# Kernel optimization log

Hardware: AMD Instinct MI355X
Metric: run time of the kernel (lower is better)

The kernel has to match this reference:

```python
import jax, jax.numpy as jnp
import numpy as np

NUM_NODES = 100000
D_IN = 64
D_OUT = 64
NUM_EDGES = 1200000


def setup_inputs() -> dict:
    key = jax.random.key(0)
    k1, k2, k3, k4 = jax.random.split(key, 4)
    features = jax.random.normal(k1, (NUM_NODES, D_IN), dtype=jnp.float32)
    edge_index = jax.random.randint(k2, (2, NUM_EDGES), 0, NUM_NODES, dtype=jnp.int64)
    # Linear(input_dim*2 -> output_dim) parameters
    W = jax.random.normal(k3, (2 * D_IN, D_OUT), dtype=jnp.float32) / np.sqrt(2 * D_IN)
    b = jax.random.normal(k4, (D_OUT,), dtype=jnp.float32) * 0.01
    return {"features": features, "edge_index": edge_index, "W": W, "b": b}


def reference(features, edge_index, W, b):
    num_nodes = features.shape[0]
    src, dst = edge_index[0], edge_index[1]
    # gather source-node features for every edge: [E, D]
    src_feats = features[src]
    # segment-sum into destination nodes (mean aggregation)
    neigh_sum = jax.ops.segment_sum(src_feats, dst, num_segments=num_nodes)
    degree = jax.ops.segment_sum(jnp.ones_like(dst, dtype=features.dtype), dst,
                                 num_segments=num_nodes)
    degree = jnp.clip(degree, 1.0)
    neigh_mean = neigh_sum / degree[:, None]
    # concat self + neighbor features, then linear (dropout = identity in eval)
    combined = jnp.concatenate([features, neigh_mean], axis=-1)
    return combined @ W + b
```

## Files before the change

### kernel.cpp

```cpp
#include <hip/hip_runtime.h>
#include <hip/hip_fp8.h>

#define N_NODES 100000
#define D 64
#define N_EDGES 1200000
#define NCB 391
#define NBLK 256
#define PAD 16
#define CHUNK ((N_EDGES + NBLK - 1) / NBLK)
#define CSR2 768

typedef __attribute__((ext_vector_type(8))) short short8v;
typedef __attribute__((ext_vector_type(4))) float f32x4;

__device__ __forceinline__ unsigned short f2bf(float x) {
    unsigned int b = __float_as_uint(x);
    b += 0x7FFFu + ((b >> 16) & 1u);
    return (unsigned short)(b >> 16);
}
__device__ __forceinline__ unsigned char ftofp8(float x) {
    __hip_fp8_e4m3 q(x);
    return (unsigned char)q.__x;
}
#if __has_builtin(__builtin_amdgcn_cvt_f32_fp8)
#define F8D(w, s) __builtin_amdgcn_cvt_f32_fp8((w), (s))
#else
__device__ __forceinline__ float f8dec(unsigned int w, unsigned int s) {
    __hip_fp8_e4m3 q; q.__x = (unsigned char)(w >> (8 * s));
    return (float)q;
}
#define F8D(w, s) f8dec((w), (s))
#endif

__global__ __launch_bounds__(256) void bin_hist(
    const int* __restrict__ eidx, int* __restrict__ hist, int* __restrict__ totP,
    const float* __restrict__ feat, unsigned char* __restrict__ f8b,
    const float* __restrict__ W, ushort* __restrict__ wb)
{
    __shared__ int h[NCB];
    for (int i = threadIdx.x; i < NCB; i += 256) h[i] = 0;
    __syncthreads();
    const int blk = blockIdx.x;

    if (blk < 32) {
        int g  = blk * 256 + threadIdx.x;
        int j  = g & 7;
        int l  = (g >> 3) & 63;
        int c4 = (g >> 9) & 3;
        int tt = g >> 11;
        int k   = 32 * tt + ((l >> 4) << 3) + j;
        int col = 16 * c4 + (l & 15);
        wb[g] = f2bf(W[k * 64 + col]);
    }

    const int beg = blk * CHUNK;
    const int end = min(beg + CHUNK, N_EDGES);
    for (int e = beg + threadIdx.x; e < end; e += 256)
        atomicAdd(&h[eidx[N_EDGES + e] >> 8], 1);

    const int total4 = N_NODES * D / 4;
    for (int i = blk * 256 + threadIdx.x; i < total4; i += NBLK * 256) {
        float4 v = ((const float4*)feat)[i];
        uchar4 o;
        o.x = ftofp8(v.x); o.y = ftofp8(v.y); o.z = ftofp8(v.z); o.w = ftofp8(v.w);
        ((uchar4*)f8b)[i] = o;
    }

    __syncthreads();
    for (int i = threadIdx.x; i < NCB; i += 256) {
        int v = h[i];
        hist[blk * NCB + i] = v;
        if (v) atomicAdd(&totP[i * PAD], v);
    }
}

__global__ __launch_bounds__(256) void rstart(
    const int* __restrict__ totP, const int* __restrict__ hist,
    int* __restrict__ boff, int* __restrict__ runstart)
{
    __shared__ int red[256];
    __shared__ int pfx[256];
    __shared__ int bo_s;

    const int tid = threadIdx.x;
    const int i   = blockIdx.x;

    int p = 0;
    for (int j = tid; j < i; j += 256) p += totP[j * PAD];
    red[tid] = p;
    __syncthreads();
    for (int off = 128; off > 0; off >>= 1) {
        if (tid < off) red[tid] += red[tid + off];
        __syncthreads();
    }
    if (tid == 0) {
        bo_s = red[0];
        boff[i] = red[0];
        if (i == 0) boff[NCB] = N_EDGES;
    }
    __syncthreads();

    int v = hist[tid * NCB + i];
    pfx[tid] = v;
    __syncthreads();
    for (int off = 1; off < 256; off <<= 1) {
        int x = (tid >= off) ? pfx[tid - off] : 0;
        __syncthreads();
        pfx[tid] += x;
        __syncthreads();
    }
    runstart[tid * NCB + i] = bo_s + pfx[tid] - v;
}

__global__ __launch_bounds__(256) void bin_fill(
    const int* __restrict__ eidx, const int* __restrict__ runstart,
    unsigned int* __restrict__ pairs)
{
    __shared__ int lcur[NCB];
    const int blk = blockIdx.x;
    for (int i = threadIdx.x; i < NCB; i += 256) lcur[i] = runstart[blk * NCB + i];
    __syncthreads();
    const int beg = blk * CHUNK;
    const int end = min(beg + CHUNK, N_EDGES);
    for (int e = beg + threadIdx.x; e < end; e += 256) {
        int src = eidx[e];
        int dst = eidx[N_EDGES + e];
        int pos = atomicAdd(&lcur[dst >> 8], 1);
        pairs[pos] = ((unsigned int)src << 8) | (unsigned int)(dst & 255);
    }
}

#define MROW 72
#define D8X(sel) (((F8D(w0.x,sel)+F8D(w1.x,sel))+(F8D(w2.x,sel)+F8D(w3.x,sel))) \
               + ((F8D(w4.x,sel)+F8D(w5.x,sel))+(F8D(w6.x,sel)+F8D(w7.x,sel))))
#define D8Y(sel) (((F8D(w0.y,sel)+F8D(w1.y,sel))+(F8D(w2.y,sel)+F8D(w3.y,sel))) \
               + ((F8D(w4.y,sel)+F8D(w5.y,sel))+(F8D(w6.y,sel)+F8D(w7.y,sel))))
#define D4X(sel) ((F8D(w0.x,sel)+F8D(w1.x,sel))+(F8D(w2.x,sel)+F8D(w3.x,sel)))
#define D4Y(sel) ((F8D(w0.y,sel)+F8D(w1.y,sel))+(F8D(w2.y,sel)+F8D(w3.y,sel)))
__global__ __launch_bounds__(256) void sage_fused(
    const unsigned char* __restrict__ f8b,
    const float* __restrict__ feat,
    const int* __restrict__ boff,
    const unsigned int* __restrict__ pairs,
    const ushort* __restrict__ wb,
    const float* __restrict__ bias,
    float* __restrict__ out)
{
    __shared__ int cnt[32];
    __shared__ int lofs[33];
    __shared__ int lcur2[32];
    __shared__ int csrL[CSR2];
    __shared__ __attribute__((aligned(16))) ushort means[32 * MROW];

    const int tid = threadIdx.x;
    const int b   = blockIdx.x >> 3;
    const int c   = blockIdx.x & 7;
    const int n0  = b * 256 + c * 32;
    if (n0 >= N_NODES) return;

    const int beg = boff[b];
    const int end = boff[b + 1];

    if (tid < 32) cnt[tid] = 0;
    __syncthreads();
    for (int j = beg + tid; j < end; j += 256) {
        unsigned int p = pairs[j];
        int ld = (int)(p & 255u);
        if ((ld >> 5) == c) atomicAdd(&cnt[ld & 31], 1);
    }
    __syncthreads();
    if (tid == 0) {
        int run = 0;
        #pragma unroll
        for (int k = 0; k < 32; ++k) { lofs[k] = run; run += cnt[k]; }
        lofs[32] = run;
    }
    __syncthreads();
    if (tid < 32) lcur2[tid] = lofs[tid];
    __syncthreads();
    for (int j = beg + tid; j < end; j += 256) {
        unsigned int p = pairs[j];
        int ld = (int)(p & 255u);
        if ((ld >> 5) == c) {
            int pos = atomicAdd(&lcur2[ld & 31], 1);
            if (pos < CSR2) csrL[pos] = (int)(p >> 8);
        }
    }
    __syncthreads();

    const int l    = tid & 7;
    const int node = tid >> 3;

    int ebeg = lofs[node];
    int eend = lofs[node + 1];
    const int deg = eend - ebeg;
    if (ebeg > CSR2) ebeg = CSR2;
    if (eend > CSR2) eend = CSR2;
    const uint2* g8 = (const uint2*)f8b;

    float s0=0.f,s1=0.f,s2=0.f,s3=0.f,s4=0.f,s5=0.f,s6=0.f,s7=0.f;
    int e = ebeg;
    for (; e + 8 <= eend; e += 8) {
        int i0=csrL[e+0], i1=csrL[e+1], i2=csrL[e+2], i3=csrL[e+3];
        int i4=csrL[e+4], i5=csrL[e+5], i6=csrL[e+6], i7=csrL[e+7];
        uint2 w0 = g8[(size_t)i0 * 8 + l];
        uint2 w1 = g8[(size_t)i1 * 8 + l];
        uint2 w2 = g8[(size_t)i2 * 8 + l];
        uint2 w3 = g8[(size_t)i3 * 8 + l];
        uint2 w4 = g8[(size_t)i4 * 8 + l];
        uint2 w5 = g8[(size_t)i5 * 8 + l];
        uint2 w6 = g8[(size_t)i6 * 8 + l];
        uint2 w7 = g8[(size_t)i7 * 8 + l];
        s0 += D8X(0); s1 += D8X(1); s2 += D8X(2); s3 += D8X(3);
        s4 += D8Y(0); s5 += D8Y(1); s6 += D8Y(2); s7 += D8Y(3);
    }
    for (; e + 4 <= eend; e += 4) {
        int i0=csrL[e+0], i1=csrL[e+1], i2=csrL[e+2], i3=csrL[e+3];
        uint2 w0 = g8[(size_t)i0 * 8 + l];
        uint2 w1 = g8[(size_t)i1 * 8 + l];
        uint2 w2 = g8[(size_t)i2 * 8 + l];
        uint2 w3 = g8[(size_t)i3 * 8 + l];
        s0 += D4X(0); s1 += D4X(1); s2 += D4X(2); s3 += D4X(3);
        s4 += D4Y(0); s5 += D4Y(1); s6 += D4Y(2); s7 += D4Y(3);
    }
    for (; e < eend; ++e) {
        uint2 w0 = g8[(size_t)csrL[e] * 8 + l];
        s0 += F8D(w0.x,0); s1 += F8D(w0.x,1); s2 += F8D(w0.x,2); s3 += F8D(w0.x,3);
        s4 += F8D(w0.y,0); s5 += F8D(w0.y,1); s6 += F8D(w0.y,2); s7 += F8D(w0.y,3);
    }

    float dg = (float)deg;
    dg = dg > 1.0f ? dg : 1.0f;
    float inv = 1.0f / dg;
    {
        ushort s[8] = { f2bf(s0*inv), f2bf(s1*inv), f2bf(s2*inv), f2bf(s3*inv),
                        f2bf(s4*inv), f2bf(s5*inv), f2bf(s6*inv), f2bf(s7*inv) };
        *(ushort4*)(means + node * MROW + l * 8)     = *(ushort4*)&s[0];
        *(ushort4*)(means + node * MROW + l * 8 + 4) = *(ushort4*)&s[4];
    }
    __syncthreads();

    const int lane = tid & 63;
    const int wv   = tid >> 6;
    const int rt   = wv >> 1;
    const int cp   = wv & 1;
    const int kg   = lane >> 4;
    const int cl   = lane & 15;

    const float* frow = feat + (size_t)(n0 + rt * 16 + cl) * 64;
    f32x4 p0 = *(const f32x4*)(frow + kg * 8);
    f32x4 p1 = *(const f32x4*)(frow + kg * 8 + 4);
    f32x4 p2 = *(const f32x4*)(frow + 32 + kg * 8);
    f32x4 p3 = *(const f32x4*)(frow + 32 + kg * 8 + 4);
    short8v a0, a1;
    #pragma unroll
    for (int k = 0; k < 4; ++k) {
        a0[k]     = (short)f2bf(p0[k]);
        a0[k + 4] = (short)f2bf(p1[k]);
        a1[k]     = (short)f2bf(p2[k]);
        a1[k + 4] = (short)f2bf(p3[k]);
    }
    const ushort* mrow = means + (rt * 16 + cl) * MROW;
    short8v a2 = *(const short8v*)(mrow + kg * 8);
    short8v a3 = *(const short8v*)(mrow + 32 + kg * 8);

    const short8v* wv8 = (const short8v*)wb;

    #pragma unroll
    for (int qq = 0; qq < 2; ++qq) {
        const int c4 = cp * 2 + qq;
        float bv = bias[c4 * 16 + cl];
        f32x4 acc = (f32x4){bv, bv, bv, bv};
        acc = __builtin_amdgcn_mfma_f32_16x16x32_bf16(
            a0, wv8[(0 * 4 + c4) * 64 + lane], acc, 0, 0, 0);
        acc = __builtin_amdgcn_mfma_f32_16x16x32_bf16(
            a1, wv8[(1 * 4 + c4) * 64 + lane], acc, 0, 0, 0);
        acc = __builtin_amdgcn_mfma_f32_16x16x32_bf16(
            a2, wv8[(2 * 4 + c4) * 64 + lane], acc, 0, 0, 0);
        acc = __builtin_amdgcn_mfma_f32_16x16x32_bf16(
            a3, wv8[(3 * 4 + c4) * 64 + lane], acc, 0, 0, 0);
        #pragma unroll
        for (int r = 0; r < 4; ++r)
            out[(size_t)(n0 + rt * 16 + kg * 4 + r) * 64 + c4 * 16 + cl] = acc[r];
    }
}

extern "C" void kernel_launch(void* const* d_in, const int* in_sizes, int n_in,
                              void* d_out, int out_size, void* d_ws, size_t ws_size,
                              hipStream_t stream) {
    const float* feat = (const float*)d_in[0];
    const int*   eidx = (const int*)d_in[1];
    const float* W    = (const float*)d_in[2];
    const float* bias = (const float*)d_in[3];
    float* out = (float*)d_out;

    int* hist     = (int*)d_ws;
    int* totP     = hist + NBLK * NCB;
    int* runstart = totP + NCB * PAD;
    int* boff     = runstart + NBLK * NCB;
    ushort* wb    = (ushort*)(boff + 396);
    unsigned int* pairs = (unsigned int*)(wb + 8192);
    unsigned char* f8b  = (unsigned char*)(pairs + N_EDGES);

    hipMemsetAsync(totP, 0, (size_t)NCB * PAD * sizeof(int), stream);

    bin_hist<<<NBLK, 256, 0, stream>>>(eidx, hist, totP, feat, f8b, W, wb);
    rstart<<<NCB, 256, 0, stream>>>(totP, hist, boff, runstart);
    bin_fill<<<NBLK, 256, 0, stream>>>(eidx, runstart, pairs);
    sage_fused<<<NCB * 8, 256, 0, stream>>>(f8b, feat, boff, pairs, wb, bias, out);
}
```

Measured before the change: 97.74 us.

## Process each 256-node bin in one 512-thread block instead of eight blocks

The fused aggregation kernel now launches one 512-thread block per 256-node bin, down from eight 256-thread blocks that each rescanned the whole bin's edge pairs and kept only their 32-node slice. The block builds a full 256-entry local CSR once, using a parallel prefix scan, then loops over four 64-node groups doing the gather-mean and the MFMA linear step. This removes the eightfold redundant reading of pairs and the atomics. The cost is a much smaller grid (391 blocks), serialized groups with extra barriers, and more shared memory, which may reduce occupancy and latency hiding.

```diff
diff --git a/kernel.cpp b/kernel.cpp
--- a/kernel.cpp
+++ b/kernel.cpp
@@ -8,7 +8,7 @@
 #define NBLK 256
 #define PAD 16
 #define CHUNK ((N_EDGES + NBLK - 1) / NBLK)
-#define CSR2 768
+#define CSRMAX 3584
 
 typedef __attribute__((ext_vector_type(8))) short short8v;
 typedef __attribute__((ext_vector_type(4))) float f32x4;
@@ -137,7 +137,7 @@
                + ((F8D(w4.y,sel)+F8D(w5.y,sel))+(F8D(w6.y,sel)+F8D(w7.y,sel))))
 #define D4X(sel) ((F8D(w0.x,sel)+F8D(w1.x,sel))+(F8D(w2.x,sel)+F8D(w3.x,sel)))
 #define D4Y(sel) ((F8D(w0.y,sel)+F8D(w1.y,sel))+(F8D(w2.y,sel)+F8D(w3.y,sel)))
-__global__ __launch_bounds__(256) void sage_fused(
+__global__ __launch_bounds__(512) void sage_fused(
     const unsigned char* __restrict__ f8b,
     const float* __restrict__ feat,
     const int* __restrict__ boff,
@@ -146,99 +146,51 @@
     const float* __restrict__ bias,
     float* __restrict__ out)
 {
-    __shared__ int cnt[32];
-    __shared__ int lofs[33];
-    __shared__ int lcur2[32];
-    __shared__ int csrL[CSR2];
-    __shared__ __attribute__((aligned(16))) ushort means[32 * MROW];
-
-    const int tid = threadIdx.x;
-    const int b   = blockIdx.x >> 3;
-    const int c   = blockIdx.x & 7;
-    const int n0  = b * 256 + c * 32;
-    if (n0 >= N_NODES) return;
-
-    const int beg = boff[b];
-    const int end = boff[b + 1];
-
-    if (tid < 32) cnt[tid] = 0;
-    __syncthreads();
-    for (int j = beg + tid; j < end; j += 256) {
+    __shared__ int cnt[256];
+    __shared__ int pfx[256];
+    __shared__ int lofs[257];
+    __shared__ int lcur[256];
+    __shared__ int csrL[CSRMAX];
+    __shared__ __attribute__((aligned(16))) ushort means[64 * MROW];
+
+    const int tid  = threadIdx.x;
+    const int b    = blockIdx.x;
+    const int base = b * 256;
+    const int beg  = boff[b];
+    const int end  = boff[b + 1];
+
+    if (tid < 256) cnt[tid] = 0;
+    __syncthreads();
+    for (int j = beg + tid; j < end; j += 512)
+        atomicAdd(&cnt[pairs[j] & 255], 1);
+    __syncthreads();
+    if (tid < 256) pfx[tid] = cnt[tid];
+    __syncthreads();
+    for (int off = 1; off < 256; off <<= 1) {
+        int x = 0;
+        if (tid < 256 && tid >= off) x = pfx[tid - off];
+        __syncthreads();
+        if (tid < 256) pfx[tid] += x;
+        __syncthreads();
+    }
+    if (tid < 256) {
+        int ex = pfx[tid] - cnt[tid];
+        lofs[tid] = ex;
+        lcur[tid] = ex;
+    }
+    if (tid == 0) lofs[256] = end - beg;
+    __syncthreads();
+    for (int j = beg + tid; j < end; j += 512) {
         unsigned int p = pairs[j];
-        int ld = (int)(p & 255u);
-        if ((ld >> 5) == c) atomicAdd(&cnt[ld & 31], 1);
-    }
-    __syncthreads();
-    if (tid == 0) {
-        int run = 0;
-        #pragma unroll
-        for (int k = 0; k < 32; ++k) { lofs[k] = run; run += cnt[k]; }
-        lofs[32] = run;
-    }
-    __syncthreads();
-    if (tid < 32) lcur2[tid] = lofs[tid];
-    __syncthreads();
-    for (int j = beg + tid; j < end; j += 256) {
-        unsigned int p = pairs[j];
-        int ld = (int)(p & 255u);
-        if ((ld >> 5) == c) {
-            int pos = atomicAdd(&lcur2[ld & 31], 1);
-            if (pos < CSR2) csrL[pos] = (int)(p >> 8);
-        }
+        int pos = atomicAdd(&lcur[p & 255], 1);
+        if (pos < CSRMAX) csrL[pos] = (int)(p >> 8);
     }
     __syncthreads();
 
     const int l    = tid & 7;
-    const int node = tid >> 3;
-
-    int ebeg = lofs[node];
-    int eend = lofs[node + 1];
-    const int deg = eend - ebeg;
-    if (ebeg > CSR2) ebeg = CSR2;
-    if (eend > CSR2) eend = CSR2;
+    const int gn8  = tid >> 3;
     const uint2* g8 = (const uint2*)f8b;
-
-    float s0=0.f,s1=0.f,s2=0.f,s3=0.f,s4=0.f,s5=0.f,s6=0.f,s7=0.f;
-    int e = ebeg;
-    for (; e + 8 <= eend; e += 8) {
-        int i0=csrL[e+0], i1=csrL[e+1], i2=csrL[e+2], i3=csrL[e+3];
-        int i4=csrL[e+4], i5=csrL[e+5], i6=csrL[e+6], i7=csrL[e+7];
-        uint2 w0 = g8[(size_t)i0 * 8 + l];
-        uint2 w1 = g8[(size_t)i1 * 8 + l];
-        uint2 w2 = g8[(size_t)i2 * 8 + l];
-        uint2 w3 = g8[(size_t)i3 * 8 + l];
-        uint2 w4 = g8[(size_t)i4 * 8 + l];
-        uint2 w5 = g8[(size_t)i5 * 8 + l];
-        uint2 w6 = g8[(size_t)i6 * 8 + l];
-        uint2 w7 = g8[(size_t)i7 * 8 + l];
-        s0 += D8X(0); s1 += D8X(1); s2 += D8X(2); s3 += D8X(3);
-        s4 += D8Y(0); s5 += D8Y(1); s6 += D8Y(2); s7 += D8Y(3);
-    }
-    for (; e + 4 <= eend; e += 4) {
-        int i0=csrL[e+0], i1=csrL[e+1], i2=csrL[e+2], i3=csrL[e+3];
-        uint2 w0 = g8[(size_t)i0 * 8 + l];
-        uint2 w1 = g8[(size_t)i1 * 8 + l];
-        uint2 w2 = g8[(size_t)i2 * 8 + l];
-        uint2 w3 = g8[(size_t)i3 * 8 + l];
-        s0 += D4X(0); s1 += D4X(1); s2 += D4X(2); s3 += D4X(3);
-        s4 += D4Y(0); s5 += D4Y(1); s6 += D4Y(2); s7 += D4Y(3);
-    }
-    for (; e < eend; ++e) {
-        uint2 w0 = g8[(size_t)csrL[e] * 8 + l];
-        s0 += F8D(w0.x,0); s1 += F8D(w0.x,1); s2 += F8D(w0.x,2); s3 += F8D(w0.x,3);
-        s4 += F8D(w0.y,0); s5 += F8D(w0.y,1); s6 += F8D(w0.y,2); s7 += F8D(w0.y,3);
-    }
-
-    float dg = (float)deg;
-    dg = dg > 1.0f ? dg : 1.0f;
-    float inv = 1.0f / dg;
-    {
-        ushort s[8] = { f2bf(s0*inv), f2bf(s1*inv), f2bf(s2*inv), f2bf(s3*inv),
-                        f2bf(s4*inv), f2bf(s5*inv), f2bf(s6*inv), f2bf(s7*inv) };
-        *(ushort4*)(means + node * MROW + l * 8)     = *(ushort4*)&s[0];
-        *(ushort4*)(means + node * MROW + l * 8 + 4) = *(ushort4*)&s[4];
-    }
-    __syncthreads();
+    const short8v* wv8 = (const short8v*)wb;
 
     const int lane = tid & 63;
     const int wv   = tid >> 6;
@@ -247,41 +199,98 @@
     const int kg   = lane >> 4;
     const int cl   = lane & 15;
 
-    const float* frow = feat + (size_t)(n0 + rt * 16 + cl) * 64;
-    f32x4 p0 = *(const f32x4*)(frow + kg * 8);
-    f32x4 p1 = *(const f32x4*)(frow + kg * 8 + 4);
-    f32x4 p2 = *(const f32x4*)(frow + 32 + kg * 8);
-    f32x4 p3 = *(const f32x4*)(frow + 32 + kg * 8 + 4);
-    short8v a0, a1;
-    #pragma unroll
-    for (int k = 0; k < 4; ++k) {
-        a0[k]     = (short)f2bf(p0[k]);
-        a0[k + 4] = (short)f2bf(p1[k]);
-        a1[k]     = (short)f2bf(p2[k]);
-        a1[k + 4] = (short)f2bf(p3[k]);
-    }
-    const ushort* mrow = means + (rt * 16 + cl) * MROW;
-    short8v a2 = *(const short8v*)(mrow + kg * 8);
-    short8v a3 = *(const short8v*)(mrow + 32 + kg * 8);
-
-    const short8v* wv8 = (const short8v*)wb;
-
-    #pragma unroll
-    for (int qq = 0; qq < 2; ++qq) {
-        const int c4 = cp * 2 + qq;
-        float bv = bias[c4 * 16 + cl];
-        f32x4 acc = (f32x4){bv, bv, bv, bv};
-        acc = __builtin_amdgcn_mfma_f32_16x16x32_bf16(
-            a0, wv8[(0 * 4 + c4) * 64 + lane], acc, 0, 0, 0);
-        acc = __builtin_amdgcn_mfma_f32_16x16x32_bf16(
-            a1, wv8[(1 * 4 + c4) * 64 + lane], acc, 0, 0, 0);
-        acc = __builtin_amdgcn_mfma_f32_16x16x32_bf16(
-            a2, wv8[(2 * 4 + c4) * 64 + lane], acc, 0, 0, 0);
-        acc = __builtin_amdgcn_mfma_f32_16x16x32_bf16(
-            a3, wv8[(3 * 4 + c4) * 64 + lane], acc, 0, 0, 0);
+    #pragma unroll 1
+    for (int g = 0; g < 4; ++g) {
+        const int ln = g * 64 + gn8;
+        int ebeg = lofs[ln];
+        int eend = lofs[ln + 1];
+        const int deg = eend - ebeg;
+        if (ebeg > CSRMAX) ebeg = CSRMAX;
+        if (eend > CSRMAX) eend = CSRMAX;
+
+        float s0=0.f,s1=0.f,s2=0.f,s3=0.f,s4=0.f,s5=0.f,s6=0.f,s7=0.f;
+        int e = ebeg;
+        for (; e + 8 <= eend; e += 8) {
+            int i0=csrL[e+0], i1=csrL[e+1], i2=csrL[e+2], i3=csrL[e+3];
+            int i4=csrL[e+4], i5=csrL[e+5], i6=csrL[e+6], i7=csrL[e+7];
+            uint2 w0 = g8[(size_t)i0 * 8 + l];
+            uint2 w1 = g8[(size_t)i1 * 8 + l];
+            uint2 w2 = g8[(size_t)i2 * 8 + l];
+            uint2 w3 = g8[(size_t)i3 * 8 + l];
+            uint2 w4 = g8[(size_t)i4 * 8 + l];
+            uint2 w5 = g8[(size_t)i5 * 8 + l];
+            uint2 w6 = g8[(size_t)i6 * 8 + l];
+            uint2 w7 = g8[(size_t)i7 * 8 + l];
+            s0 += D8X(0); s1 += D8X(1); s2 += D8X(2); s3 += D8X(3);
+            s4 += D8Y(0); s5 += D8Y(1); s6 += D8Y(2); s7 += D8Y(3);
+        }
+        for (; e + 4 <= eend; e += 4) {
+            int i0=csrL[e+0], i1=csrL[e+1], i2=csrL[e+2], i3=csrL[e+3];
+            uint2 w0 = g8[(size_t)i0 * 8 + l];
+            uint2 w1 = g8[(size_t)i1 * 8 + l];
+            uint2 w2 = g8[(size_t)i2 * 8 + l];
+            uint2 w3 = g8[(size_t)i3 * 8 + l];
+            s0 += D4X(0); s1 += D4X(1); s2 += D4X(2); s3 += D4X(3);
+            s4 += D4Y(0); s5 += D4Y(1); s6 += D4Y(2); s7 += D4Y(3);
+        }
+        for (; e < eend; ++e) {
+            uint2 w0 = g8[(size_t)csrL[e] * 8 + l];
+            s0 += F8D(w0.x,0); s1 += F8D(w0.x,1); s2 += F8D(w0.x,2); s3 += F8D(w0.x,3);
+            s4 += F8D(w0.y,0); s5 += F8D(w0.y,1); s6 += F8D(w0.y,2); s7 += F8D(w0.y,3);
+        }
+
+        float dg = (float)deg;
+        dg = dg > 1.0f ? dg : 1.0f;
+        float inv = 1.0f / dg;
+        {
+            ushort s[8] = { f2bf(s0*inv), f2bf(s1*inv), f2bf(s2*inv), f2bf(s3*inv),
+                            f2bf(s4*inv), f2bf(s5*inv), f2bf(s6*inv), f2bf(s7*inv) };
+            *(ushort4*)(means + gn8 * MROW + l * 8)     = *(ushort4*)&s[0];
+            *(ushort4*)(means + gn8 * MROW + l * 8 + 4) = *(ushort4*)&s[4];
+        }
+        __syncthreads();
+
+        const int n0g = base + g * 64;
+        const int nA  = n0g + rt * 16 + cl;
+        const int nAc = nA < N_NODES ? nA : N_NODES - 1;
+        const float* frow = feat + (size_t)nAc * 64;
+        f32x4 p0 = *(const f32x4*)(frow + kg * 8);
+        f32x4 p1 = *(const f32x4*)(frow + kg * 8 + 4);
+        f32x4 p2 = *(const f32x4*)(frow + 32 + kg * 8);
+        f32x4 p3 = *(const f32x4*)(frow + 32 + kg * 8 + 4);
+        short8v a0, a1;
         #pragma unroll
-        for (int r = 0; r < 4; ++r)
-            out[(size_t)(n0 + rt * 16 + kg * 4 + r) * 64 + c4 * 16 + cl] = acc[r];
+        for (int k = 0; k < 4; ++k) {
+            a0[k]     = (short)f2bf(p0[k]);
+            a0[k + 4] = (short)f2bf(p1[k]);
+            a1[k]     = (short)f2bf(p2[k]);
+            a1[k + 4] = (short)f2bf(p3[k]);
+        }
+        const ushort* mrow = means + (rt * 16 + cl) * MROW;
+        short8v a2 = *(const short8v*)(mrow + kg * 8);
+        short8v a3 = *(const short8v*)(mrow + 32 + kg * 8);
+
+        #pragma unroll
+        for (int qq = 0; qq < 2; ++qq) {
+            const int c4 = cp * 2 + qq;
+            float bv = bias[c4 * 16 + cl];
+            f32x4 acc = (f32x4){bv, bv, bv, bv};
+            acc = __builtin_amdgcn_mfma_f32_16x16x32_bf16(
+                a0, wv8[(0 * 4 + c4) * 64 + lane], acc, 0, 0, 0);
+            acc = __builtin_amdgcn_mfma_f32_16x16x32_bf16(
+                a1, wv8[(1 * 4 + c4) * 64 + lane], acc, 0, 0, 0);
+            acc = __builtin_amdgcn_mfma_f32_16x16x32_bf16(
+                a2, wv8[(2 * 4 + c4) * 64 + lane], acc, 0, 0, 0);
+            acc = __builtin_amdgcn_mfma_f32_16x16x32_bf16(
+                a3, wv8[(3 * 4 + c4) * 64 + lane], acc, 0, 0, 0);
+            #pragma unroll
+            for (int r = 0; r < 4; ++r) {
+                int orow = n0g + rt * 16 + kg * 4 + r;
+                if (orow < N_NODES)
+                    out[(size_t)orow * 64 + c4 * 16 + cl] = acc[r];
+            }
+        }
+        __syncthreads();
     }
 }
 
@@ -307,5 +316,5 @@
     bin_hist<<<NBLK, 256, 0, stream>>>(eidx, hist, totP, feat, f8b, W, wb);
     rstart<<<NCB, 256, 0, stream>>>(totP, hist, boff, runstart);
     bin_fill<<<NBLK, 256, 0, stream>>>(eidx, runstart, pairs);
-    sage_fused<<<NCB * 8, 256, 0, stream>>>(f8b, feat, boff, pairs, wb, bias, out);
-}
+    sage_fused<<<NCB, 512, 0, stream>>>(f8b, feat, boff, pairs, wb, bias, out);
+}
```

New measurement: 86.91 us, median of 2. 11.1% less time.
